# Kernel tuning notes

Measured on AMD Instinct MI355X. Metric: run time of the kernel, lower is better.

Reference implementation:

```python
import jax, jax.numpy as jnp
import numpy as np

M = 100000   # BS*L nodes
D_IN = 256   # in_d
D_OUT = 256  # out_d
E = 1024     # number of edges; indices index the out_d axis (faithful to source quirk)


def setup_inputs() -> dict:
    key = jax.random.key(0)
    k1, k2, k3 = jax.random.split(key, 3)
    node_features = jax.random.normal(k1, (1, M, D_IN), dtype=jnp.float32)
    W = jax.random.normal(k2, (D_OUT, D_IN), dtype=jnp.float32) * (1.0 / np.sqrt(D_IN))
    b = jnp.zeros((D_OUT,), dtype=jnp.float32)
    edge_mapping = jax.random.randint(k3, (2, E), 0, D_OUT, dtype=jnp.int64)
    batch_lens = jnp.ones((M, 1), dtype=jnp.float32)
    return {"node_features": node_features, "W": W, "b": b,
            "edge_mapping": edge_mapping, "batch_lens": batch_lens}


def reference(node_features, W, b, edge_mapping, batch_lens):
    # fc: [1, M, in_d] -> [1, M, out_d]
    h = jnp.einsum('bmi,oi->bmo', node_features, W) + b
    residual = h                              # [1, M, D_OUT]
    hf = jnp.swapaxes(h, 1, 2)[0]             # [D_OUT, M]  (transpose(2,1).squeeze(0))
    gathered = hf[edge_mapping[1]]            # [E, M]      (index_select dim=0)
    agg = jnp.zeros_like(hf).at[edge_mapping[0]].add(gathered)  # scatter-add, [D_OUT, M]
    new_nf = agg.T                            # [M, D_OUT]
    out = (new_nf + residual) / batch_lens    # broadcast -> [1, M, D_OUT]
    return out
```

## Files before the change

### kernel.cpp

```cpp
#include <hip/hip_runtime.h>
#include <cstdint>

constexpr int D = 256;
constexpr int TM = 128;

typedef __bf16 bf16x8 __attribute__((ext_vector_type(8)));
typedef float  f32x4  __attribute__((ext_vector_type(4)));

__global__ void prep_copy(const float* __restrict__ W, const float* __restrict__ b,
                          float* __restrict__ W2, float* __restrict__ b2) {
    int i = blockIdx.x * 256 + threadIdx.x;
    W2[i] = W[i];
    if (blockIdx.x == 0) b2[threadIdx.x] = b[threadIdx.x];
}

__global__ void prep_edges(const int* __restrict__ em, int E,
                           const float* __restrict__ W, const float* __restrict__ b,
                           float* __restrict__ W2, float* __restrict__ b2) {
    int e = blockIdx.x;
    int k = threadIdx.x;
    int dst = em[e];
    int src = em[E + e];
    atomicAdd(&W2[dst * D + k], W[src * D + k]);
    if (k == 0) atomicAdd(&b2[dst], b[src]);
}

__global__ void prep_convert(const float* __restrict__ W2, ushort* __restrict__ Wh,
                             ushort* __restrict__ Wl) {
    int i = blockIdx.x * 256 + threadIdx.x;
    int o = i >> 8, k = i & 255;
    float x = W2[i];
    uint32_t u  = __float_as_uint(x);
    uint32_t hu = u & 0xFFFF0000u;
    float r = x - __uint_as_float(hu);
    uint32_t ru = __float_as_uint(r);
    uint32_t lu = ru + 0x7FFFu + ((ru >> 16) & 1u);
    int kc = k >> 5, kk = k & 31, q = kk >> 3, j = kk & 7;
    int o16b = o >> 4;
    int lane = (o & 15) + 16 * q;
    int idx = kc * 8192 + (o16b * 64 + lane) * 8 + j;
    Wh[idx] = (ushort)(hu >> 16);
    Wl[idx] = (ushort)(lu >> 16);
}

__device__ __forceinline__ void gl_lds16(const ushort* g, ushort* l) {
    __builtin_amdgcn_global_load_lds(
        (const __attribute__((address_space(1))) uint32_t*)g,
        (__attribute__((address_space(3))) uint32_t*)l, 16, 0, 0);
}

__device__ __forceinline__ void cvt8(const float4& f0, const float4& f1,
                                     uint4& hi, uint4& lo) {
    float xs[8] = {f0.x, f0.y, f0.z, f0.w, f1.x, f1.y, f1.z, f1.w};
    uint32_t h[8], l[8];
    #pragma unroll
    for (int j = 0; j < 8; ++j) {
        uint32_t u  = __float_as_uint(xs[j]);
        uint32_t hu = u & 0xFFFF0000u;
        h[j] = hu;
        float r = xs[j] - __uint_as_float(hu);
        uint32_t ru = __float_as_uint(r);
        l[j] = ru + 0x7FFFu + ((ru >> 16) & 1u);
    }
    hi = make_uint4((h[0] >> 16) | (h[1] & 0xFFFF0000u),
                    (h[2] >> 16) | (h[3] & 0xFFFF0000u),
                    (h[4] >> 16) | (h[5] & 0xFFFF0000u),
                    (h[6] >> 16) | (h[7] & 0xFFFF0000u));
    lo = make_uint4((l[0] >> 16) | (l[1] & 0xFFFF0000u),
                    (l[2] >> 16) | (l[3] & 0xFFFF0000u),
                    (l[4] >> 16) | (l[5] & 0xFFFF0000u),
                    (l[6] >> 16) | (l[7] & 0xFFFF0000u));
}

__global__ __launch_bounds__(256, 2) void resgcn_mfma(
    const float* __restrict__ X, const ushort* __restrict__ Whg,
    const ushort* __restrict__ Wlg, const float* __restrict__ b2,
    const float* __restrict__ blen, float* __restrict__ out, int M)
{
    __shared__ ushort Xh[8][64][8];
    __shared__ ushort Xl[8][64][8];
    __shared__ ushort Wh[16][64][8];
    __shared__ ushort Wl[16][64][8];

    const int tid  = threadIdx.x;
    const int lane = tid & 63;
    const int wv   = tid >> 6;
    const int m0   = blockIdx.x * TM;

    const int sm = tid >> 1;
    const int sh = tid & 1;
    int srow = m0 + sm; if (srow >= M) srow = M - 1;
    const float* xrow = X + (size_t)srow * D + sh * 16;
    const int m16b = sm >> 4;
    const int mlow = sm & 15;

    f32x4 acc[8][4];
    #pragma unroll
    for (int a = 0; a < 8; ++a)
        #pragma unroll
        for (int b = 0; b < 4; ++b) acc[a][b] = (f32x4){0.f, 0.f, 0.f, 0.f};

    for (int kc = 0; kc < 8; ++kc) {
        __syncthreads();

        {
            const ushort* gh = Whg + kc * 8192;
            const ushort* gl = Wlg + kc * 8192;
            ushort* lh = &Wh[0][0][0];
            ushort* ll = &Wl[0][0][0];
            #pragma unroll
            for (int i = 0; i < 4; ++i) {
                int off = (i * 256 + tid) * 8;
                gl_lds16(gh + off, lh + off);
                gl_lds16(gl + off, ll + off);
            }
        }

        {
            const float* p = xrow + kc * 32;
            float4 f0 = *(const float4*)(p + 0);
            float4 f1 = *(const float4*)(p + 4);
            float4 f2 = *(const float4*)(p + 8);
            float4 f3 = *(const float4*)(p + 12);
            uint4 h0, l0, h1, l1;
            cvt8(f0, f1, h0, l0);
            cvt8(f2, f3, h1, l1);
            const int q0 = sh * 2, q1 = sh * 2 + 1;
            *(uint4*)&Xh[m16b][mlow + 16 * q0][0] = h0;
            *(uint4*)&Xl[m16b][mlow + 16 * q0][0] = l0;
            *(uint4*)&Xh[m16b][mlow + 16 * q1][0] = h1;
            *(uint4*)&Xl[m16b][mlow + 16 * q1][0] = l1;
        }

        __syncthreads();

        bf16x8 bh[4], blo[4];
        #pragma unroll
        for (int b = 0; b < 4; ++b) {
            bh[b]  = *(const bf16x8*)&Wh[wv * 4 + b][lane][0];
            blo[b] = *(const bf16x8*)&Wl[wv * 4 + b][lane][0];
        }
        #pragma unroll
        for (int a = 0; a < 8; ++a) {
            bf16x8 ah = *(const bf16x8*)&Xh[a][lane][0];
            bf16x8 al = *(const bf16x8*)&Xl[a][lane][0];
            #pragma unroll
            for (int b = 0; b < 4; ++b) {
                acc[a][b] = __builtin_amdgcn_mfma_f32_16x16x32_bf16(ah, bh[b],  acc[a][b], 0, 0, 0);
                acc[a][b] = __builtin_amdgcn_mfma_f32_16x16x32_bf16(al, bh[b],  acc[a][b], 0, 0, 0);
                acc[a][b] = __builtin_amdgcn_mfma_f32_16x16x32_bf16(ah, blo[b], acc[a][b], 0, 0, 0);
            }
        }
    }

    const int col = lane & 15;
    const int rq  = lane >> 4;
    float bias[4];
    #pragma unroll
    for (int b = 0; b < 4; ++b) bias[b] = b2[(wv * 4 + b) * 16 + col];

    #pragma unroll
    for (int a = 0; a < 8; ++a) {
        #pragma unroll
        for (int r = 0; r < 4; ++r) {
            int m = m0 + a * 16 + rq * 4 + r;
            if (m < M) {
                float inv = 1.0f / blen[m];
                #pragma unroll
                for (int b = 0; b < 4; ++b) {
                    int o = (wv * 4 + b) * 16 + col;
                    out[(size_t)m * D + o] = (acc[a][b][r] + bias[b]) * inv;
                }
            }
        }
    }
}

extern "C" void kernel_launch(void* const* d_in, const int* in_sizes, int n_in,
                              void* d_out, int out_size, void* d_ws, size_t ws_size,
                              hipStream_t stream) {
    (void)n_in; (void)out_size; (void)ws_size;
    const float* X  = (const float*)d_in[0];
    const float* W  = (const float*)d_in[1];
    const float* b  = (const float*)d_in[2];
    const int*   em = (const int*)d_in[3];
    const float* bl = (const float*)d_in[4];
    float* out = (float*)d_out;

    const int M = in_sizes[0] / D;
    const int E = in_sizes[3] / 2;

    float*  W2 = (float*)d_ws;
    float*  b2 = W2 + D * D;
    ushort* Wh = (ushort*)(b2 + D);
    ushort* Wl = Wh + D * D;

    prep_copy<<<D * D / 256, 256, 0, stream>>>(W, b, W2, b2);
    prep_edges<<<E, D, 0, stream>>>(em, E, W, b, W2, b2);
    prep_convert<<<D * D / 256, 256, 0, stream>>>(W2, Wh, Wl);

    int mblocks = (M + TM - 1) / TM;
    resgcn_mfma<<<mblocks, 256, 0, stream>>>(X, Wh, Wl, b2, bl, out, M);
}
```

Before: 217.7 us.

## Fuse weight prep into one kernel and double-buffer X tiles with register-held W

The three prep kernels (copy, atomic edge scatter, bf16 split) become one kernel in which each block owns an output row and scans every edge, so the atomics and two launches go away. The main GEMM no longer stages W through LDS; each wave loads its hi/lo W fragments straight from global into registers and prefetches the next k-chunk. X tiles are double-buffered in LDS so the next chunk's load and conversion overlap the current MFMAs, leaving one barrier per iteration. Costs are more register pressure and a serial E-length loop per prep block.

```diff
diff --git a/kernel.cpp b/kernel.cpp
--- a/kernel.cpp
+++ b/kernel.cpp
@@ -7,46 +7,31 @@
 typedef __bf16 bf16x8 __attribute__((ext_vector_type(8)));
 typedef float  f32x4  __attribute__((ext_vector_type(4)));
 
-__global__ void prep_copy(const float* __restrict__ W, const float* __restrict__ b,
-                          float* __restrict__ W2, float* __restrict__ b2) {
-    int i = blockIdx.x * 256 + threadIdx.x;
-    W2[i] = W[i];
-    if (blockIdx.x == 0) b2[threadIdx.x] = b[threadIdx.x];
-}
-
-__global__ void prep_edges(const int* __restrict__ em, int E,
-                           const float* __restrict__ W, const float* __restrict__ b,
-                           float* __restrict__ W2, float* __restrict__ b2) {
-    int e = blockIdx.x;
-    int k = threadIdx.x;
-    int dst = em[e];
-    int src = em[E + e];
-    atomicAdd(&W2[dst * D + k], W[src * D + k]);
-    if (k == 0) atomicAdd(&b2[dst], b[src]);
-}
-
-__global__ void prep_convert(const float* __restrict__ W2, ushort* __restrict__ Wh,
-                             ushort* __restrict__ Wl) {
-    int i = blockIdx.x * 256 + threadIdx.x;
-    int o = i >> 8, k = i & 255;
-    float x = W2[i];
-    uint32_t u  = __float_as_uint(x);
+__global__ void prep_kernel(const float* __restrict__ W, const float* __restrict__ b,
+                            const int* __restrict__ em, int E,
+                            ushort* __restrict__ Wh, ushort* __restrict__ Wl,
+                            float* __restrict__ b2) {
+    const int o = blockIdx.x;
+    const int k = threadIdx.x;
+    float acc  = W[o * D + k];
+    float bacc = b[o];
+    for (int e = 0; e < E; ++e) {
+        if (em[e] == o) {
+            int src = em[E + e];
+            acc  += W[src * D + k];
+            bacc += b[src];
+        }
+    }
+    uint32_t u  = __float_as_uint(acc);
     uint32_t hu = u & 0xFFFF0000u;
-    float r = x - __uint_as_float(hu);
+    float r = acc - __uint_as_float(hu);
     uint32_t ru = __float_as_uint(r);
     uint32_t lu = ru + 0x7FFFu + ((ru >> 16) & 1u);
     int kc = k >> 5, kk = k & 31, q = kk >> 3, j = kk & 7;
-    int o16b = o >> 4;
-    int lane = (o & 15) + 16 * q;
-    int idx = kc * 8192 + (o16b * 64 + lane) * 8 + j;
+    int idx = kc * 8192 + (((o >> 4) * 4 + q) * 16 + (o & 15)) * 8 + j;
     Wh[idx] = (ushort)(hu >> 16);
     Wl[idx] = (ushort)(lu >> 16);
-}
-
-__device__ __forceinline__ void gl_lds16(const ushort* g, ushort* l) {
-    __builtin_amdgcn_global_load_lds(
-        (const __attribute__((address_space(1))) uint32_t*)g,
-        (__attribute__((address_space(3))) uint32_t*)l, 16, 0, 0);
+    if (k == 0) b2[o] = bacc;
 }
 
 __device__ __forceinline__ void cvt8(const float4& f0, const float4& f1,
@@ -77,14 +62,12 @@
     const ushort* __restrict__ Wlg, const float* __restrict__ b2,
     const float* __restrict__ blen, float* __restrict__ out, int M)
 {
-    __shared__ ushort Xh[8][64][8];
-    __shared__ ushort Xl[8][64][8];
-    __shared__ ushort Wh[16][64][8];
-    __shared__ ushort Wl[16][64][8];
+    __shared__ alignas(16) ushort Xh[2][8][64][8];
+    __shared__ alignas(16) ushort Xl[2][8][64][8];
 
     const int tid  = threadIdx.x;
     const int lane = tid & 63;
-    const int wv   = tid >> 6;
+    const int w    = tid >> 6;
     const int m0   = blockIdx.x * TM;
 
     const int sm = tid >> 1;
@@ -93,6 +76,10 @@
     const float* xrow = X + (size_t)srow * D + sh * 16;
     const int m16b = sm >> 4;
     const int mlow = sm & 15;
+    const int q0 = sh * 2, q1 = sh * 2 + 1;
+
+    const ushort* bbase_h = Whg + ((size_t)(w * 4) * 64 + lane) * 8;
+    const ushort* bbase_l = Wlg + ((size_t)(w * 4) * 64 + lane) * 8;
 
     f32x4 acc[8][4];
     #pragma unroll
@@ -100,64 +87,79 @@
         #pragma unroll
         for (int b = 0; b < 4; ++b) acc[a][b] = (f32x4){0.f, 0.f, 0.f, 0.f};
 
+    bf16x8 bh[4], bl[4], nbh[4], nbl[4];
+
+    {
+        float4 f0 = *(const float4*)(xrow + 0);
+        float4 f1 = *(const float4*)(xrow + 4);
+        float4 f2 = *(const float4*)(xrow + 8);
+        float4 f3 = *(const float4*)(xrow + 12);
+        uint4 h0, l0, h1, l1;
+        cvt8(f0, f1, h0, l0);
+        cvt8(f2, f3, h1, l1);
+        *(uint4*)&Xh[0][m16b][mlow + 16 * q0][0] = h0;
+        *(uint4*)&Xl[0][m16b][mlow + 16 * q0][0] = l0;
+        *(uint4*)&Xh[0][m16b][mlow + 16 * q1][0] = h1;
+        *(uint4*)&Xl[0][m16b][mlow + 16 * q1][0] = l1;
+    }
+    #pragma unroll
+    for (int b = 0; b < 4; ++b) {
+        bh[b] = *(const bf16x8*)(bbase_h + b * 512);
+        bl[b] = *(const bf16x8*)(bbase_l + b * 512);
+    }
+    __syncthreads();
+
+    #pragma unroll 2
     for (int kc = 0; kc < 8; ++kc) {
-        __syncthreads();
-
-        {
-            const ushort* gh = Whg + kc * 8192;
-            const ushort* gl = Wlg + kc * 8192;
-            ushort* lh = &Wh[0][0][0];
-            ushort* ll = &Wl[0][0][0];
+        const int buf = kc & 1;
+
+        float4 f0, f1, f2, f3;
+        if (kc < 7) {
+            const float* p = xrow + (kc + 1) * 32;
+            f0 = *(const float4*)(p + 0);
+            f1 = *(const float4*)(p + 4);
+            f2 = *(const float4*)(p + 8);
+            f3 = *(const float4*)(p + 12);
+            const ushort* gh = bbase_h + (size_t)(kc + 1) * 8192;
+            const ushort* gl = bbase_l + (size_t)(kc + 1) * 8192;
             #pragma unroll
-            for (int i = 0; i < 4; ++i) {
-                int off = (i * 256 + tid) * 8;
-                gl_lds16(gh + off, lh + off);
-                gl_lds16(gl + off, ll + off);
+            for (int b = 0; b < 4; ++b) {
+                nbh[b] = *(const bf16x8*)(gh + b * 512);
+                nbl[b] = *(const bf16x8*)(gl + b * 512);
             }
         }
 
-        {
-            const float* p = xrow + kc * 32;
-            float4 f0 = *(const float4*)(p + 0);
-            float4 f1 = *(const float4*)(p + 4);
-            float4 f2 = *(const float4*)(p + 8);
-            float4 f3 = *(const float4*)(p + 12);
+        #pragma unroll
+        for (int a = 0; a < 8; ++a) {
+            bf16x8 ah = *(const bf16x8*)&Xh[buf][a][lane][0];
+            bf16x8 al = *(const bf16x8*)&Xl[buf][a][lane][0];
+            #pragma unroll
+            for (int b = 0; b < 4; ++b) {
+                acc[a][b] = __builtin_amdgcn_mfma_f32_16x16x32_bf16(ah, bh[b], acc[a][b], 0, 0, 0);
+                acc[a][b] = __builtin_amdgcn_mfma_f32_16x16x32_bf16(al, bh[b], acc[a][b], 0, 0, 0);
+                acc[a][b] = __builtin_amdgcn_mfma_f32_16x16x32_bf16(ah, bl[b], acc[a][b], 0, 0, 0);
+            }
+        }
+
+        if (kc < 7) {
             uint4 h0, l0, h1, l1;
             cvt8(f0, f1, h0, l0);
             cvt8(f2, f3, h1, l1);
-            const int q0 = sh * 2, q1 = sh * 2 + 1;
-            *(uint4*)&Xh[m16b][mlow + 16 * q0][0] = h0;
-            *(uint4*)&Xl[m16b][mlow + 16 * q0][0] = l0;
-            *(uint4*)&Xh[m16b][mlow + 16 * q1][0] = h1;
-            *(uint4*)&Xl[m16b][mlow + 16 * q1][0] = l1;
-        }
-
+            *(uint4*)&Xh[buf ^ 1][m16b][mlow + 16 * q0][0] = h0;
+            *(uint4*)&Xl[buf ^ 1][m16b][mlow + 16 * q0][0] = l0;
+            *(uint4*)&Xh[buf ^ 1][m16b][mlow + 16 * q1][0] = h1;
+            *(uint4*)&Xl[buf ^ 1][m16b][mlow + 16 * q1][0] = l1;
+            #pragma unroll
+            for (int b = 0; b < 4; ++b) { bh[b] = nbh[b]; bl[b] = nbl[b]; }
+        }
         __syncthreads();
-
-        bf16x8 bh[4], blo[4];
-        #pragma unroll
-        for (int b = 0; b < 4; ++b) {
-            bh[b]  = *(const bf16x8*)&Wh[wv * 4 + b][lane][0];
-            blo[b] = *(const bf16x8*)&Wl[wv * 4 + b][lane][0];
-        }
-        #pragma unroll
-        for (int a = 0; a < 8; ++a) {
-            bf16x8 ah = *(const bf16x8*)&Xh[a][lane][0];
-            bf16x8 al = *(const bf16x8*)&Xl[a][lane][0];
-            #pragma unroll
-            for (int b = 0; b < 4; ++b) {
-                acc[a][b] = __builtin_amdgcn_mfma_f32_16x16x32_bf16(ah, bh[b],  acc[a][b], 0, 0, 0);
-                acc[a][b] = __builtin_amdgcn_mfma_f32_16x16x32_bf16(al, bh[b],  acc[a][b], 0, 0, 0);
-                acc[a][b] = __builtin_amdgcn_mfma_f32_16x16x32_bf16(ah, blo[b], acc[a][b], 0, 0, 0);
-            }
-        }
     }
 
     const int col = lane & 15;
     const int rq  = lane >> 4;
     float bias[4];
     #pragma unroll
-    for (int b = 0; b < 4; ++b) bias[b] = b2[(wv * 4 + b) * 16 + col];
+    for (int b = 0; b < 4; ++b) bias[b] = b2[(w * 4 + b) * 16 + col];
 
     #pragma unroll
     for (int a = 0; a < 8; ++a) {
@@ -168,7 +170,7 @@
                 float inv = 1.0f / blen[m];
                 #pragma unroll
                 for (int b = 0; b < 4; ++b) {
-                    int o = (wv * 4 + b) * 16 + col;
+                    int o = (w * 4 + b) * 16 + col;
                     out[(size_t)m * D + o] = (acc[a][b][r] + bias[b]) * inv;
                 }
             }
@@ -190,14 +192,11 @@
     const int M = in_sizes[0] / D;
     const int E = in_sizes[3] / 2;
 
-    float*  W2 = (float*)d_ws;
-    float*  b2 = W2 + D * D;
-    ushort* Wh = (ushort*)(b2 + D);
+    ushort* Wh = (ushort*)d_ws;
     ushort* Wl = Wh + D * D;
-
-    prep_copy<<<D * D / 256, 256, 0, stream>>>(W, b, W2, b2);
-    prep_edges<<<E, D, 0, stream>>>(em, E, W, b, W2, b2);
-    prep_convert<<<D * D / 256, 256, 0, stream>>>(W2, Wh, Wl);
+    float*  b2 = (float*)(Wl + D * D);
+
+    prep_kernel<<<D, D, 0, stream>>>(W, b, em, E, Wh, Wl, b2);
 
     int mblocks = (M + TM - 1) / TM;
     resgcn_mfma<<<mblocks, 256, 0, stream>>>(X, Wh, Wl, b2, bl, out, M);
```

Result: slower. 276.5 us (+27.0%).

## Drop LDS staging, load MFMA operands directly with register prefetch, split output columns

Applied to the files above, without the earlier changes.

The GEMM kernel no longer stages X and W through shared memory. Each wave loads its A fragments (fp32 X, converted to bf16 hi/lo in registers) and B fragments (pre-swizzled bf16 W) straight from global memory, and prefetches the next K chunk into registers, so all __syncthreads disappear. The W low-part correction term is dropped, cutting MFMAs from 3 to 2 per tile, though this lowers weight precision to plain bf16. The grid doubles to split the output columns across two blocks, which means each X row tile is read twice from global memory.

```diff
diff --git a/kernel.cpp b/kernel.cpp
--- a/kernel.cpp
+++ b/kernel.cpp
@@ -2,7 +2,6 @@
 #include <cstdint>
 
 constexpr int D = 256;
-constexpr int TM = 128;
 
 typedef __bf16 bf16x8 __attribute__((ext_vector_type(8)));
 typedef float  f32x4  __attribute__((ext_vector_type(4)));
@@ -25,32 +24,18 @@
     if (k == 0) atomicAdd(&b2[dst], b[src]);
 }
 
-__global__ void prep_convert(const float* __restrict__ W2, ushort* __restrict__ Wh,
-                             ushort* __restrict__ Wl) {
+__global__ void prep_convert(const float* __restrict__ W2, ushort* __restrict__ Wh) {
     int i = blockIdx.x * 256 + threadIdx.x;
     int o = i >> 8, k = i & 255;
-    float x = W2[i];
-    uint32_t u  = __float_as_uint(x);
-    uint32_t hu = u & 0xFFFF0000u;
-    float r = x - __uint_as_float(hu);
-    uint32_t ru = __float_as_uint(r);
-    uint32_t lu = ru + 0x7FFFu + ((ru >> 16) & 1u);
+    uint32_t u = __float_as_uint(W2[i]);
+    uint32_t r = u + 0x7FFFu + ((u >> 16) & 1u);
     int kc = k >> 5, kk = k & 31, q = kk >> 3, j = kk & 7;
-    int o16b = o >> 4;
-    int lane = (o & 15) + 16 * q;
-    int idx = kc * 8192 + (o16b * 64 + lane) * 8 + j;
-    Wh[idx] = (ushort)(hu >> 16);
-    Wl[idx] = (ushort)(lu >> 16);
-}
-
-__device__ __forceinline__ void gl_lds16(const ushort* g, ushort* l) {
-    __builtin_amdgcn_global_load_lds(
-        (const __attribute__((address_space(1))) uint32_t*)g,
-        (__attribute__((address_space(3))) uint32_t*)l, 16, 0, 0);
+    int idx = kc * 8192 + (((o >> 4) * 4 + q) * 16 + (o & 15)) * 8 + j;
+    Wh[idx] = (ushort)(r >> 16);
 }
 
 __device__ __forceinline__ void cvt8(const float4& f0, const float4& f1,
-                                     uint4& hi, uint4& lo) {
+                                     bf16x8& hi8, bf16x8& lo8) {
     float xs[8] = {f0.x, f0.y, f0.z, f0.w, f1.x, f1.y, f1.z, f1.w};
     uint32_t h[8], l[8];
     #pragma unroll
@@ -62,94 +47,92 @@
         uint32_t ru = __float_as_uint(r);
         l[j] = ru + 0x7FFFu + ((ru >> 16) & 1u);
     }
-    hi = make_uint4((h[0] >> 16) | (h[1] & 0xFFFF0000u),
-                    (h[2] >> 16) | (h[3] & 0xFFFF0000u),
-                    (h[4] >> 16) | (h[5] & 0xFFFF0000u),
-                    (h[6] >> 16) | (h[7] & 0xFFFF0000u));
-    lo = make_uint4((l[0] >> 16) | (l[1] & 0xFFFF0000u),
-                    (l[2] >> 16) | (l[3] & 0xFFFF0000u),
-                    (l[4] >> 16) | (l[5] & 0xFFFF0000u),
-                    (l[6] >> 16) | (l[7] & 0xFFFF0000u));
+    uint4 hp = make_uint4((h[0] >> 16) | (h[1] & 0xFFFF0000u),
+                          (h[2] >> 16) | (h[3] & 0xFFFF0000u),
+                          (h[4] >> 16) | (h[5] & 0xFFFF0000u),
+                          (h[6] >> 16) | (h[7] & 0xFFFF0000u));
+    uint4 lp = make_uint4((l[0] >> 16) | (l[1] & 0xFFFF0000u),
+                          (l[2] >> 16) | (l[3] & 0xFFFF0000u),
+                          (l[4] >> 16) | (l[5] & 0xFFFF0000u),
+                          (l[6] >> 16) | (l[7] & 0xFFFF0000u));
+    hi8 = *(bf16x8*)&hp;
+    lo8 = *(bf16x8*)&lp;
 }
 
-__global__ __launch_bounds__(256, 2) void resgcn_mfma(
+__global__ __launch_bounds__(256) void resgcn_mfma(
     const float* __restrict__ X, const ushort* __restrict__ Whg,
-    const ushort* __restrict__ Wlg, const float* __restrict__ b2,
-    const float* __restrict__ blen, float* __restrict__ out, int M)
+    const float* __restrict__ b2, const float* __restrict__ blen,
+    float* __restrict__ out, int M)
 {
-    __shared__ ushort Xh[8][64][8];
-    __shared__ ushort Xl[8][64][8];
-    __shared__ ushort Wh[16][64][8];
-    __shared__ ushort Wl[16][64][8];
-
     const int tid  = threadIdx.x;
     const int lane = tid & 63;
-    const int wv   = tid >> 6;
-    const int m0   = blockIdx.x * TM;
+    const int w    = tid >> 6;
+    const int wm   = w >> 1;
+    const int wo   = w & 1;
+    const int bid  = blockIdx.x;
+    const int ob   = bid & 1;
+    const int mb   = bid >> 1;
 
-    const int sm = tid >> 1;
-    const int sh = tid & 1;
-    int srow = m0 + sm; if (srow >= M) srow = M - 1;
-    const float* xrow = X + (size_t)srow * D + sh * 16;
-    const int m16b = sm >> 4;
-    const int mlow = sm & 15;
+    const int m0 = mb * 128 + wm * 64;
+    const int ob16 = ob * 8 + wo * 4;
 
-    f32x4 acc[8][4];
+    const float* pA[4];
     #pragma unroll
-    for (int a = 0; a < 8; ++a)
+    for (int a = 0; a < 4; ++a) {
+        int r = m0 + a * 16 + (lane & 15);
+        if (r >= M) r = M - 1;
+        pA[a] = X + (size_t)r * D + ((lane >> 4) * 8);
+    }
+    const ushort* pB = Whg + ((size_t)ob16 * 64 + lane) * 8;
+
+    f32x4 acc[4][4];
+    #pragma unroll
+    for (int a = 0; a < 4; ++a)
         #pragma unroll
         for (int b = 0; b < 4; ++b) acc[a][b] = (f32x4){0.f, 0.f, 0.f, 0.f};
 
+    float4 xa[4][2];
+    bf16x8 bf[4];
+    #pragma unroll
+    for (int a = 0; a < 4; ++a) {
+        xa[a][0] = *(const float4*)(pA[a]);
+        xa[a][1] = *(const float4*)(pA[a] + 4);
+    }
+    #pragma unroll
+    for (int b = 0; b < 4; ++b) bf[b] = *(const bf16x8*)(pB + b * 512);
+
     for (int kc = 0; kc < 8; ++kc) {
-        __syncthreads();
-
-        {
-            const ushort* gh = Whg + kc * 8192;
-            const ushort* gl = Wlg + kc * 8192;
-            ushort* lh = &Wh[0][0][0];
-            ushort* ll = &Wl[0][0][0];
+        float4 nxa[4][2];
+        bf16x8 nbf[4];
+        if (kc < 7) {
             #pragma unroll
-            for (int i = 0; i < 4; ++i) {
-                int off = (i * 256 + tid) * 8;
-                gl_lds16(gh + off, lh + off);
-                gl_lds16(gl + off, ll + off);
+            for (int a = 0; a < 4; ++a) {
+                const float* p = pA[a] + (kc + 1) * 32;
+                nxa[a][0] = *(const float4*)(p);
+                nxa[a][1] = *(const float4*)(p + 4);
             }
+            const ushort* q = pB + (size_t)(kc + 1) * 8192;
+            #pragma unroll
+            for (int b = 0; b < 4; ++b) nbf[b] = *(const bf16x8*)(q + b * 512);
         }
 
-        {
-            const float* p = xrow + kc * 32;
-            float4 f0 = *(const float4*)(p + 0);
-            float4 f1 = *(const float4*)(p + 4);
-            float4 f2 = *(const float4*)(p + 8);
-            float4 f3 = *(const float4*)(p + 12);
-            uint4 h0, l0, h1, l1;
-            cvt8(f0, f1, h0, l0);
-            cvt8(f2, f3, h1, l1);
-            const int q0 = sh * 2, q1 = sh * 2 + 1;
-            *(uint4*)&Xh[m16b][mlow + 16 * q0][0] = h0;
-            *(uint4*)&Xl[m16b][mlow + 16 * q0][0] = l0;
-            *(uint4*)&Xh[m16b][mlow + 16 * q1][0] = h1;
-            *(uint4*)&Xl[m16b][mlow + 16 * q1][0] = l1;
-        }
+        bf16x8 ah[4], al[4];
+        #pragma unroll
+        for (int a = 0; a < 4; ++a) cvt8(xa[a][0], xa[a][1], ah[a], al[a]);
 
-        __syncthreads();
-
-        bf16x8 bh[4], blo[4];
         #pragma unroll
-        for (int b = 0; b < 4; ++b) {
-            bh[b]  = *(const bf16x8*)&Wh[wv * 4 + b][lane][0];
-            blo[b] = *(const bf16x8*)&Wl[wv * 4 + b][lane][0];
-        }
-        #pragma unroll
-        for (int a = 0; a < 8; ++a) {
-            bf16x8 ah = *(const bf16x8*)&Xh[a][lane][0];
-            bf16x8 al = *(const bf16x8*)&Xl[a][lane][0];
+        for (int a = 0; a < 4; ++a)
             #pragma unroll
             for (int b = 0; b < 4; ++b) {
-                acc[a][b] = __builtin_amdgcn_mfma_f32_16x16x32_bf16(ah, bh[b],  acc[a][b], 0, 0, 0);
-                acc[a][b] = __builtin_amdgcn_mfma_f32_16x16x32_bf16(al, bh[b],  acc[a][b], 0, 0, 0);
-                acc[a][b] = __builtin_amdgcn_mfma_f32_16x16x32_bf16(ah, blo[b], acc[a][b], 0, 0, 0);
+                acc[a][b] = __builtin_amdgcn_mfma_f32_16x16x32_bf16(ah[a], bf[b], acc[a][b], 0, 0, 0);
+                acc[a][b] = __builtin_amdgcn_mfma_f32_16x16x32_bf16(al[a], bf[b], acc[a][b], 0, 0, 0);
             }
+
+        if (kc < 7) {
+            #pragma unroll
+            for (int a = 0; a < 4; ++a) { xa[a][0] = nxa[a][0]; xa[a][1] = nxa[a][1]; }
+            #pragma unroll
+            for (int b = 0; b < 4; ++b) bf[b] = nbf[b];
         }
     }
 
@@ -157,10 +140,10 @@
     const int rq  = lane >> 4;
     float bias[4];
     #pragma unroll
-    for (int b = 0; b < 4; ++b) bias[b] = b2[(wv * 4 + b) * 16 + col];
+    for (int b = 0; b < 4; ++b) bias[b] = b2[(ob16 + b) * 16 + col];
 
     #pragma unroll
-    for (int a = 0; a < 8; ++a) {
+    for (int a = 0; a < 4; ++a) {
         #pragma unroll
         for (int r = 0; r < 4; ++r) {
             int m = m0 + a * 16 + rq * 4 + r;
@@ -168,7 +151,7 @@
                 float inv = 1.0f / blen[m];
                 #pragma unroll
                 for (int b = 0; b < 4; ++b) {
-                    int o = (wv * 4 + b) * 16 + col;
+                    int o = (ob16 + b) * 16 + col;
                     out[(size_t)m * D + o] = (acc[a][b][r] + bias[b]) * inv;
                 }
             }
@@ -193,12 +176,11 @@
     float*  W2 = (float*)d_ws;
     float*  b2 = W2 + D * D;
     ushort* Wh = (ushort*)(b2 + D);
-    ushort* Wl = Wh + D * D;
 
     prep_copy<<<D * D / 256, 256, 0, stream>>>(W, b, W2, b2);
     prep_edges<<<E, D, 0, stream>>>(em, E, W, b, W2, b2);
-    prep_convert<<<D * D / 256, 256, 0, stream>>>(W2, Wh, Wl);
+    prep_convert<<<D * D / 256, 256, 0, stream>>>(W2, Wh);
 
-    int mblocks = (M + TM - 1) / TM;
-    resgcn_mfma<<<mblocks, 256, 0, stream>>>(X, Wh, Wl, b2, bl, out, M);
+    int mblocks = (M + 127) / 128;
+    resgcn_mfma<<<mblocks * 2, 256, 0, stream>>>(X, Wh, b2, bl, out, M);
 }
```

Measured after the change: 232.3 us. 6.7% more time.
